# Optimization experiments

Hardware: AMD Instinct MI355X
Metric: run time of the kernel (lower is better)

## Reference

```python
import jax, jax.numpy as jnp
import numpy as np

B, T, E, D = 8, 2048, 1024, 64  # batch, seq, embed_dim, head_dim

def setup_inputs() -> dict:
    key = jax.random.key(0)
    kx, kq, kk, kv = jax.random.split(key, 4)
    scale = 1.0 / np.sqrt(E)
    return {
        "x": jax.random.normal(kx, (B, T, E), dtype=jnp.float32),
        "Wq": jax.random.normal(kq, (E, D), dtype=jnp.float32) * scale,
        "Wk": jax.random.normal(kk, (E, D), dtype=jnp.float32) * scale,
        "Wv": jax.random.normal(kv, (E, D), dtype=jnp.float32) * scale,
    }

def reference(x, Wq, Wk, Wv):
    # single-head causal attention (dropout in eval mode = identity)
    q = jnp.einsum('bte,ed->btd', x, Wq)
    k = jnp.einsum('bte,ed->btd', x, Wk)
    v = jnp.einsum('bte,ed->btd', x, Wv)
    head_dim = q.shape[-1]
    wei = jnp.einsum('btd,bsd->bts', q, k) * (head_dim ** -0.5)  # [B,T,T]
    causal = jnp.tril(jnp.ones((wei.shape[1], wei.shape[2]), dtype=bool))
    wei = jnp.where(causal, wei, -jnp.inf)
    wei = jax.nn.softmax(wei, axis=-1)
    out = jnp.einsum('bts,bsd->btd', wei, v)  # [B,T,D]
    return out
```

## Files before the change

### kernel.cpp

```cpp
#include <hip/hip_runtime.h>
#include <hip/hip_bf16.h>
#include <cstdint>
#include <cstddef>

#define B_ 8
#define T_ 2048
#define E_ 1024
#define D_ 64

typedef __attribute__((ext_vector_type(8))) short bf16x8;
typedef __attribute__((ext_vector_type(4))) float f32x4;
typedef __attribute__((ext_vector_type(16))) float f32x16;
typedef __attribute__((ext_vector_type(4))) unsigned short u16x4;

#define QSCALE 0.1803368801111204f

__device__ __forceinline__ short f2bf(float f){
    __hip_bfloat16 h = __float2bfloat16(f);
    return *reinterpret_cast<short*>(&h);
}

__device__ __forceinline__ bf16x8 cvt8v(const f32x4 a, const f32x4 b){
    bf16x8 r;
    r[0]=f2bf(a[0]); r[1]=f2bf(a[1]); r[2]=f2bf(a[2]); r[3]=f2bf(a[3]);
    r[4]=f2bf(b[0]); r[5]=f2bf(b[1]); r[6]=f2bf(b[2]); r[7]=f2bf(b[3]);
    return r;
}

__global__ __launch_bounds__(256) void wconv_kernel(
    const float* __restrict__ Wq, const float* __restrict__ Wk,
    const float* __restrict__ Wv, __hip_bfloat16* __restrict__ Wfrag)
{
    const int g = blockIdx.x*256 + threadIdx.x;
    const int l = g & 63;
    const int ntg = (g >> 6) % 6;
    const int cg = g / 384;
    const int n = ntg*32 + (l & 31);
    const int m = n >> 6;
    const int ncol = n & 63;
    const float* W = (m==0) ? Wq : (m==1) ? Wk : Wv;
    const float sc = (m==0) ? QSCALE : 1.0f;
    const int k0 = cg*16 + (l>>5)*8;
    bf16x8 r;
    #pragma unroll
    for (int j=0;j<8;++j)
        r[j] = f2bf(W[(size_t)(k0+j)*64 + ncol] * sc);
    *reinterpret_cast<bf16x8*>(Wfrag + (size_t)g*8) = r;
}

__global__ __launch_bounds__(384, 3) void proj_kernel(
    const float* __restrict__ x, const __hip_bfloat16* __restrict__ Wfrag,
    __hip_bfloat16* __restrict__ Qo, __hip_bfloat16* __restrict__ Ko,
    __hip_bfloat16* __restrict__ VTg)
{
    __shared__ __align__(16) unsigned short xs[2][32*64];
    __shared__ float vt[32*65];
    const int tid = threadIdx.x;
    const int w = tid>>6, l = tid&63;
    const int l31 = l&31, kg = l>>5;
    const float* xp = x + (size_t)blockIdx.x*32*E_;

    f32x16 acc;
    #pragma unroll
    for (int j=0;j<16;++j) acc[j]=0.f;

    const bf16x8* Wfp = reinterpret_cast<const bf16x8*>(Wfrag);

    bf16x8 btA[4], btB[4];
    #pragma unroll
    for (int c=0;c<4;++c)
        btA[c] = Wfp[(size_t)(((0*4+c)*6 + w)*64 + l)];

    const int srow = tid>>3, sc8 = tid&7;

    if (tid < 256){
        f32x4 v0 = *reinterpret_cast<const f32x4*>(xp + (size_t)srow*E_ + sc8*8);
        f32x4 v1 = *reinterpret_cast<const f32x4*>(xp + (size_t)srow*E_ + sc8*8 + 4);
        *reinterpret_cast<bf16x8*>((char*)&xs[0][0] + srow*128 + ((sc8*16) ^ ((srow&7)<<4))) = cvt8v(v0, v1);
    }
    __syncthreads();

#define PSTEP(T, BC, BN)                                                       \
    {                                                                          \
        const int t = (T);                                                     \
        if (t+1 < 16){                                                         \
            _Pragma("unroll")                                                  \
            for (int c=0;c<4;++c)                                              \
                BN[c] = Wfp[(size_t)((((t+1)*4+c)*6 + w)*64 + l)];             \
        }                                                                      \
        f32x4 xa0, xa1;                                                        \
        if (t+1 < 16 && tid < 256){                                            \
            xa0 = *reinterpret_cast<const f32x4*>(xp + (size_t)srow*E_ + (t+1)*64 + sc8*8);     \
            xa1 = *reinterpret_cast<const f32x4*>(xp + (size_t)srow*E_ + (t+1)*64 + sc8*8 + 4); \
        }                                                                      \
        const char* xb = (const char*)&xs[t&1][0];                             \
        _Pragma("unroll")                                                      \
        for (int c=0;c<4;++c){                                                 \
            bf16x8 af = *reinterpret_cast<const bf16x8*>(xb + l31*128 + (((c*32 + kg*16)) ^ ((l31&7)<<4))); \
            acc = __builtin_amdgcn_mfma_f32_32x32x16_bf16(af, BC[c], acc, 0,0,0); \
        }                                                                      \
        if (t+1 < 16){                                                         \
            if (tid < 256)                                                     \
                *reinterpret_cast<bf16x8*>((char*)&xs[(t+1)&1][0] + srow*128 + ((sc8*16) ^ ((srow&7)<<4))) = cvt8v(xa0, xa1); \
            __syncthreads();                                                   \
        }                                                                      \
    }

    for (int t2=0; t2<8; ++t2){
        PSTEP(2*t2,   btA, btB)
        PSTEP(2*t2+1, btB, btA)
    }
#undef PSTEP

    const size_t rowBase = (size_t)blockIdx.x*32;
    const int mat = w>>1;
    const int col = (w&1)*32 + l31;
    if (mat < 2){
        __hip_bfloat16* dst = (mat==0) ? Qo : Ko;
        #pragma unroll
        for (int reg=0; reg<16; ++reg){
            const int mr = (reg&3) + 8*(reg>>2) + 4*kg;
            dst[(rowBase + mr)*64 + col] = __float2bfloat16(acc[reg]);
        }
    }
    if (mat == 2){
        #pragma unroll
        for (int reg=0; reg<16; ++reg){
            const int mr = (reg&3) + 8*(reg>>2) + 4*kg;
            vt[mr*65 + col] = acc[reg];
        }
    }
    __syncthreads();
    if (tid < 256){
        const int bb = blockIdx.x >> 6;
        const int t0 = (blockIdx.x & 63)*32;
        const int d = tid>>2, rseg = tid&3;
        bf16x8 pk;
        #pragma unroll
        for (int j=0;j<8;++j)
            pk[j] = f2bf(vt[(rseg*8+j)*65 + d]);
        *reinterpret_cast<bf16x8*>(VTg + (size_t)bb*64*T_ + (size_t)d*T_ + t0 + rseg*8) = pk;
    }
}

__global__ __launch_bounds__(256) void repack_kernel(
    const __hip_bfloat16* __restrict__ Qb, const __hip_bfloat16* __restrict__ Kb,
    const __hip_bfloat16* __restrict__ VTb,
    __hip_bfloat16* __restrict__ Qfrag, __hip_bfloat16* __restrict__ Kfrag,
    __hip_bfloat16* __restrict__ Vfrag)
{
    const int blk = blockIdx.x;
    const int tid = threadIdx.x;
    if (blk < 512){
        const int g = blk*256 + tid;
        const int l = g & 63, ks = (g>>6)&1, nt = (g>>7)&3, t = (g>>9)&31, b = g>>14;
        const int l15 = l&15, lg = l>>4;
        bf16x8 v = *reinterpret_cast<const bf16x8*>(
            Kb + ((size_t)b*T_ + t*64 + nt*16 + l15)*64 + ks*32 + lg*8);
        *reinterpret_cast<bf16x8*>(Kfrag + (size_t)g*8) = v;
    } else if (blk < 1024){
        const int g = (blk-512)*256 + tid;
        const int l = g & 63, ks = (g>>6)&1, dt = (g>>7)&3, t = (g>>9)&31, b = g>>14;
        const int l15 = l&15, lg = l>>4;
        bf16x8 v = *reinterpret_cast<const bf16x8*>(
            VTb + (size_t)b*64*T_ + (size_t)(dt*16 + l15)*T_ + t*64 + ks*32 + lg*8);
        *reinterpret_cast<bf16x8*>(Vfrag + (size_t)g*8) = v;
    } else {
        const int g = (blk-1024)*256 + tid;
        const int l = g & 63, ks = (g>>6)&1, s = (g>>7)&127, b = g>>14;
        const int l15 = l&15, lg = l>>4;
        bf16x8 v = *reinterpret_cast<const bf16x8*>(
            Qb + ((size_t)b*T_ + s*16 + l15)*64 + ks*32 + lg*8);
        *reinterpret_cast<bf16x8*>(Qfrag + (size_t)g*8) = v;
    }
}

__global__ __launch_bounds__(256, 2) void fattn_kernel(
    const __hip_bfloat16* __restrict__ Qfrag, const __hip_bfloat16* __restrict__ Kfrag,
    const __hip_bfloat16* __restrict__ Vfrag, float* __restrict__ out)
{
    __shared__ __align__(16) unsigned short Pl[4][16*64];
    __shared__ float Morg[4][2][16];
    __shared__ float Lorg[4][2][16];
    __shared__ __align__(16) float Oorg[4][2][16*64];

    const int tid = threadIdx.x;
    const int w = tid>>6, l = tid&63;
    const int l15 = l&15, lg = l>>4;

    const int b = blockIdx.x & 7;
    const int p = blockIdx.x >> 3;
    const int sA = p, sB = 127 - p;
    const int nA = (sA>>2) + 1, nB = (sB>>2) + 1;
    const int NU = nA + nB;
    const size_t batchoff = (size_t)b * T_ * 64;

    const bf16x8* qfp = reinterpret_cast<const bf16x8*>(Qfrag);
    const bf16x8* kfp = reinterpret_cast<const bf16x8*>(Kfrag);
    const bf16x8* vfp = reinterpret_cast<const bf16x8*>(Vfrag);
    char* pw = (char*)&Pl[w][0];

    const int qrA = sA*16 + l15, qrB = sB*16 + l15;
    const bf16x8 qA0 = qfp[(size_t)((b*128 + sA)*2 + 0)*64 + l];
    const bf16x8 qA1 = qfp[(size_t)((b*128 + sA)*2 + 1)*64 + l];
    const bf16x8 qB0 = qfp[(size_t)((b*128 + sB)*2 + 0)*64 + l];
    const bf16x8 qB1 = qfp[(size_t)((b*128 + sB)*2 + 1)*64 + l];

    f32x4 oA[4], oB[4];
    #pragma unroll
    for (int i=0;i<4;++i){ oA[i] = (f32x4){0.f,0.f,0.f,0.f}; oB[i] = (f32x4){0.f,0.f,0.f,0.f}; }
    float mA = -1e30f, lA = 0.f, mB = -1e30f, lB = 0.f;

    bf16x8 kf[8], vf[8];

    {
        const int u0 = w;
        const int kvt = (u0 < nA ? u0 : u0 - nA);
        #pragma unroll
        for (int ks=0;ks<2;++ks)
            #pragma unroll
            for (int nt=0;nt<4;++nt)
                kf[ks*4+nt] = kfp[(size_t)(((b*32 + kvt)*4 + nt)*2 + ks)*64 + l];
    }

    auto body = [&](f32x4 (&o)[4], float &mrun, float &lrun,
                    const bf16x8 &qf0, const bf16x8 &qf1,
                    int qrow, int kv0, bool diag, bool hasN, int kvtn)
    {
        f32x4 s4[4];
        #pragma unroll
        for (int nt=0;nt<4;++nt) s4[nt] = (f32x4){0.f,0.f,0.f,0.f};
        __builtin_amdgcn_s_setprio(1);
        #pragma unroll
        for (int ks=0;ks<2;++ks){
            const bf16x8 qf = ks ? qf1 : qf0;
            #pragma unroll
            for (int nt=0;nt<4;++nt)
                s4[nt] = __builtin_amdgcn_mfma_f32_16x16x32_bf16(kf[ks*4+nt], qf, s4[nt], 0,0,0);
        }
        __builtin_amdgcn_s_setprio(0);

        if (hasN){
            #pragma unroll
            for (int ks=0;ks<2;++ks)
                #pragma unroll
                for (int nt=0;nt<4;++nt)
                    kf[ks*4+nt] = kfp[(size_t)(((b*32 + kvtn)*4 + nt)*2 + ks)*64 + l];
        }

        if (diag){
            #pragma unroll
            for (int nt=0;nt<4;++nt)
                #pragma unroll
                for (int rr=0;rr<4;++rr){
                    const int kv = kv0 + nt*16 + lg*4 + rr;
                    if (kv > qrow) s4[nt][rr] = -1e30f;
                }
        }

        float pm;
        {
            float m0 = fmaxf(fmaxf(s4[0][0],s4[0][1]), fmaxf(s4[0][2],s4[0][3]));
            float m1 = fmaxf(fmaxf(s4[1][0],s4[1][1]), fmaxf(s4[1][2],s4[1][3]));
            float m2 = fmaxf(fmaxf(s4[2][0],s4[2][1]), fmaxf(s4[2][2],s4[2][3]));
            float m3 = fmaxf(fmaxf(s4[3][0],s4[3][1]), fmaxf(s4[3][2],s4[3][3]));
            pm = fmaxf(fmaxf(m0,m1), fmaxf(m2,m3));
        }
        pm = fmaxf(pm, __shfl_xor(pm, 16));
        pm = fmaxf(pm, __shfl_xor(pm, 32));
        if (pm > mrun + 8.0f){
            const float scl = exp2f(mrun - pm);
            mrun = pm; lrun *= scl;
            #pragma unroll
            for (int dt=0;dt<4;++dt)
                #pragma unroll
                for (int j=0;j<4;++j) o[dt][j] *= scl;
        }
        float rs = 0.f;
        #pragma unroll
        for (int nt=0;nt<4;++nt)
            #pragma unroll
            for (int rr=0;rr<4;++rr){
                const float pv = exp2f(s4[nt][rr] - mrun);
                s4[nt][rr] = pv; rs += pv;
            }
        rs += __shfl_xor(rs, 16);
        rs += __shfl_xor(rs, 32);
        lrun += rs;

        #pragma unroll
        for (int nt=0;nt<4;++nt){
            u16x4 pk;
            #pragma unroll
            for (int rr=0;rr<4;++rr) pk[rr] = (unsigned short)f2bf(s4[nt][rr]);
            *reinterpret_cast<u16x4*>(pw + l15*128 + ((nt*32 + lg*8) ^ ((l15&7)<<4))) = pk;
        }

        __builtin_amdgcn_s_setprio(1);
        #pragma unroll
        for (int ks=0;ks<2;++ks){
            bf16x8 pf = *reinterpret_cast<const bf16x8*>(pw + l15*128 + ((ks*64 + lg*16) ^ ((l15&7)<<4)));
            #pragma unroll
            for (int dt=0;dt<4;++dt)
                o[dt] = __builtin_amdgcn_mfma_f32_16x16x32_bf16(vf[ks*4+dt], pf, o[dt], 0,0,0);
        }
        __builtin_amdgcn_s_setprio(0);
    };

    for (int u = w; u < NU; u += 4){
        const bool isA = (u < nA);
        const int kvt = isA ? u : (u - nA);
        const int kv0 = kvt*64;
        const bool diag = isA ? (kvt == nA-1) : (kvt == nB-1);

        #pragma unroll
        for (int ks=0;ks<2;++ks)
            #pragma unroll
            for (int dt=0;dt<4;++dt)
                vf[ks*4+dt] = vfp[(size_t)(((b*32 + kvt)*4 + dt)*2 + ks)*64 + l];

        const int un = u + 4;
        const bool hasN = un < NU;
        const int kvtn = hasN ? (un < nA ? un : un - nA) : 0;

        if (isA) body(oA, mA, lA, qA0, qA1, qrA, kv0, diag, hasN, kvtn);
        else     body(oB, mB, lB, qB0, qB1, qrB, kv0, diag, hasN, kvtn);
    }

    #pragma unroll
    for (int dt=0;dt<4;++dt){
        *reinterpret_cast<f32x4*>(&Oorg[w][0][l15*64 + dt*16 + lg*4]) = oA[dt];
        *reinterpret_cast<f32x4*>(&Oorg[w][1][l15*64 + dt*16 + lg*4]) = oB[dt];
    }
    if (lg == 0){
        Morg[w][0][l15] = mA; Lorg[w][0][l15] = lA;
        Morg[w][1][l15] = mB; Lorg[w][1][l15] = lB;
    }
    __syncthreads();
    {
        const int h = tid>>7, q = (tid>>3)&15, d0 = (tid&7)*8;
        const float m0=Morg[0][h][q], m1=Morg[1][h][q], m2=Morg[2][h][q], m3=Morg[3][h][q];
        const float M = fmaxf(fmaxf(m0,m1), fmaxf(m2,m3));
        const float a0=exp2f(m0-M), a1=exp2f(m1-M), a2=exp2f(m2-M), a3=exp2f(m3-M);
        const float L = a0*Lorg[0][h][q] + a1*Lorg[1][h][q] + a2*Lorg[2][h][q] + a3*Lorg[3][h][q];
        const float inv = 1.0f / L;
        const int s = h ? sB : sA;
        float* op = out + batchoff + (size_t)(s*16 + q)*64 + d0;
        #pragma unroll
        for (int j=0;j<8;++j){
            const float v = a0*Oorg[0][h][q*64+d0+j] + a1*Oorg[1][h][q*64+d0+j]
                          + a2*Oorg[2][h][q*64+d0+j] + a3*Oorg[3][h][q*64+d0+j];
            op[j] = v * inv;
        }
    }
}

extern "C" void kernel_launch(void* const* d_in, const int* in_sizes, int n_in,
                              void* d_out, int out_size, void* d_ws, size_t ws_size,
                              hipStream_t stream) {
    const float* x  = (const float*)d_in[0];
    const float* Wq = (const float*)d_in[1];
    const float* Wk = (const float*)d_in[2];
    const float* Wv = (const float*)d_in[3];
    float* out = (float*)d_out;

    const size_t NTOK = (size_t)B_*T_*64;
    __hip_bfloat16* Wfrag = (__hip_bfloat16*)d_ws;
    __hip_bfloat16* Qb    = Wfrag + (size_t)24576*8;
    __hip_bfloat16* Kb    = Qb + NTOK;
    __hip_bfloat16* VTb   = Kb + NTOK;
    __hip_bfloat16* Qfrag = VTb + NTOK;
    __hip_bfloat16* Kfrag = Qfrag + NTOK;
    __hip_bfloat16* Vfrag = Kfrag + NTOK;

    wconv_kernel<<<96, 256, 0, stream>>>(Wq, Wk, Wv, Wfrag);
    proj_kernel<<<512, 384, 0, stream>>>(x, Wfrag, Qb, Kb, VTb);
    repack_kernel<<<1536, 256, 0, stream>>>(Qb, Kb, VTb, Qfrag, Kfrag, Vfrag);
    fattn_kernel<<<512, 256, 0, stream>>>(Qfrag, Kfrag, Vfrag, out);
}
```

Measured before the change: 44.16 us.

## Fuse Q/K/V fragment repacking into projection kernel epilogue

The projection kernel now stages all three Q, K and V accumulator tiles in shared memory and writes them out directly in the MFMA fragment layouts that the attention kernel consumes. This removes the separate repack kernel launch and the intermediate row-major Q/K and transposed V buffers, along with their global write and re-read. In exchange it uses more LDS per block (three padded 32x65 float tiles), which may lower occupancy of the projection kernel, and the epilogue writes are smaller and more scattered.

```diff
diff --git a/kernel.cpp b/kernel.cpp
--- a/kernel.cpp
+++ b/kernel.cpp
@@ -50,11 +50,13 @@
 
 __global__ __launch_bounds__(384, 3) void proj_kernel(
     const float* __restrict__ x, const __hip_bfloat16* __restrict__ Wfrag,
-    __hip_bfloat16* __restrict__ Qo, __hip_bfloat16* __restrict__ Ko,
-    __hip_bfloat16* __restrict__ VTg)
+    __hip_bfloat16* __restrict__ Qfrag, __hip_bfloat16* __restrict__ Kfrag,
+    __hip_bfloat16* __restrict__ Vfrag)
 {
     __shared__ __align__(16) unsigned short xs[2][32*64];
-    __shared__ float vt[32*65];
+    __shared__ float vtQ[32*65];
+    __shared__ float vtK[32*65];
+    __shared__ float vtV[32*65];
     const int tid = threadIdx.x;
     const int w = tid>>6, l = tid&63;
     const int l31 = l&31, kg = l>>5;
@@ -112,66 +114,48 @@
     }
 #undef PSTEP
 
-    const size_t rowBase = (size_t)blockIdx.x*32;
-    const int mat = w>>1;
-    const int col = (w&1)*32 + l31;
-    if (mat < 2){
-        __hip_bfloat16* dst = (mat==0) ? Qo : Ko;
+    {
+        float* vtX = (w<2) ? vtQ : (w<4) ? vtK : vtV;
+        const int col = (w&1)*32 + l31;
         #pragma unroll
         for (int reg=0; reg<16; ++reg){
             const int mr = (reg&3) + 8*(reg>>2) + 4*kg;
-            dst[(rowBase + mr)*64 + col] = __float2bfloat16(acc[reg]);
-        }
-    }
-    if (mat == 2){
-        #pragma unroll
-        for (int reg=0; reg<16; ++reg){
-            const int mr = (reg&3) + 8*(reg>>2) + 4*kg;
-            vt[mr*65 + col] = acc[reg];
+            vtX[mr*65 + col] = acc[reg];
         }
     }
     __syncthreads();
     if (tid < 256){
-        const int bb = blockIdx.x >> 6;
-        const int t0 = (blockIdx.x & 63)*32;
-        const int d = tid>>2, rseg = tid&3;
-        bf16x8 pk;
-        #pragma unroll
-        for (int j=0;j<8;++j)
-            pk[j] = f2bf(vt[(rseg*8+j)*65 + d]);
-        *reinterpret_cast<bf16x8*>(VTg + (size_t)bb*64*T_ + (size_t)d*T_ + t0 + rseg*8) = pk;
-    }
-}
-
-__global__ __launch_bounds__(256) void repack_kernel(
-    const __hip_bfloat16* __restrict__ Qb, const __hip_bfloat16* __restrict__ Kb,
-    const __hip_bfloat16* __restrict__ VTb,
-    __hip_bfloat16* __restrict__ Qfrag, __hip_bfloat16* __restrict__ Kfrag,
-    __hip_bfloat16* __restrict__ Vfrag)
-{
-    const int blk = blockIdx.x;
-    const int tid = threadIdx.x;
-    if (blk < 512){
-        const int g = blk*256 + tid;
-        const int l = g & 63, ks = (g>>6)&1, nt = (g>>7)&3, t = (g>>9)&31, b = g>>14;
-        const int l15 = l&15, lg = l>>4;
-        bf16x8 v = *reinterpret_cast<const bf16x8*>(
-            Kb + ((size_t)b*T_ + t*64 + nt*16 + l15)*64 + ks*32 + lg*8);
-        *reinterpret_cast<bf16x8*>(Kfrag + (size_t)g*8) = v;
-    } else if (blk < 1024){
-        const int g = (blk-512)*256 + tid;
-        const int l = g & 63, ks = (g>>6)&1, dt = (g>>7)&3, t = (g>>9)&31, b = g>>14;
-        const int l15 = l&15, lg = l>>4;
-        bf16x8 v = *reinterpret_cast<const bf16x8*>(
-            VTb + (size_t)b*64*T_ + (size_t)(dt*16 + l15)*T_ + t*64 + ks*32 + lg*8);
-        *reinterpret_cast<bf16x8*>(Vfrag + (size_t)g*8) = v;
-    } else {
-        const int g = (blk-1024)*256 + tid;
-        const int l = g & 63, ks = (g>>6)&1, s = (g>>7)&127, b = g>>14;
-        const int l15 = l&15, lg = l>>4;
-        bf16x8 v = *reinterpret_cast<const bf16x8*>(
-            Qb + ((size_t)b*T_ + s*16 + l15)*64 + ks*32 + lg*8);
-        *reinterpret_cast<bf16x8*>(Qfrag + (size_t)g*8) = v;
+        const int q = blockIdx.x, b = q>>6, q63 = q&63, t = q63>>1;
+        const int su  = (tid>>7)&1, ksw = (tid>>6)&1, lw = tid&63;
+        const int lw15 = lw&15, lwg = lw>>4;
+        {
+            f32x4 a0, a1;
+            #pragma unroll
+            for (int j=0;j<4;++j) a0[j] = vtQ[(su*16+lw15)*65 + ksw*32 + lwg*8 + j];
+            #pragma unroll
+            for (int j=0;j<4;++j) a1[j] = vtQ[(su*16+lw15)*65 + ksw*32 + lwg*8 + 4 + j];
+            const size_t gi = ((size_t)(b*128 + 2*q63 + su)*2 + ksw)*64 + lw;
+            *reinterpret_cast<bf16x8*>(Qfrag + gi*8) = cvt8v(a0, a1);
+        }
+        {
+            f32x4 a0, a1;
+            #pragma unroll
+            for (int j=0;j<4;++j) a0[j] = vtK[(su*16+lw15)*65 + ksw*32 + lwg*8 + j];
+            #pragma unroll
+            for (int j=0;j<4;++j) a1[j] = vtK[(su*16+lw15)*65 + ksw*32 + lwg*8 + 4 + j];
+            const int nt = (q&1)*2 + su;
+            const size_t gi = (((size_t)(b*32 + t)*4 + nt)*2 + ksw)*64 + lw;
+            *reinterpret_cast<bf16x8*>(Kfrag + gi*8) = cvt8v(a0, a1);
+        }
+        {
+            const int dt = tid>>6;
+            bf16x8 pk;
+            #pragma unroll
+            for (int j=0;j<8;++j)
+                pk[j] = f2bf(vtV[(lwg*8+j)*65 + dt*16 + lw15]);
+            const size_t gi = (((size_t)(b*32 + t)*4 + dt)*2 + (q&1))*64 + lw;
+            *reinterpret_cast<bf16x8*>(Vfrag + gi*8) = pk;
+        }
     }
 }
 
@@ -366,15 +350,11 @@
 
     const size_t NTOK = (size_t)B_*T_*64;
     __hip_bfloat16* Wfrag = (__hip_bfloat16*)d_ws;
-    __hip_bfloat16* Qb    = Wfrag + (size_t)24576*8;
-    __hip_bfloat16* Kb    = Qb + NTOK;
-    __hip_bfloat16* VTb   = Kb + NTOK;
-    __hip_bfloat16* Qfrag = VTb + NTOK;
+    __hip_bfloat16* Qfrag = Wfrag + (size_t)24576*8;
     __hip_bfloat16* Kfrag = Qfrag + NTOK;
     __hip_bfloat16* Vfrag = Kfrag + NTOK;
 
     wconv_kernel<<<96, 256, 0, stream>>>(Wq, Wk, Wv, Wfrag);
-    proj_kernel<<<512, 384, 0, stream>>>(x, Wfrag, Qb, Kb, VTb);
-    repack_kernel<<<1536, 256, 0, stream>>>(Qb, Kb, VTb, Qfrag, Kfrag, Vfrag);
+    proj_kernel<<<512, 384, 0, stream>>>(x, Wfrag, Qfrag, Kfrag, Vfrag);
     fattn_kernel<<<512, 256, 0, stream>>>(Qfrag, Kfrag, Vfrag, out);
 }
```

New measurement: 41.27 us. -6.5%, faster.
